# Kernel optimization log

Hardware: AMD Instinct MI355X
Metric: run time of the kernel (lower is better)

Reference implementation:

```python
import jax, jax.numpy as jnp
import numpy as np

B, L, E, H, D = 4, 4096, 1024, 16, 64  # batch, seq, embed, heads, head_dim
EPS = 1e-6


def setup_inputs() -> dict:
    key = jax.random.key(0)
    k1, k2, k3 = jax.random.split(key, 3)
    return {
        "q": jax.random.normal(k1, (B, L, E), dtype=jnp.float32),
        "k": jax.random.normal(k2, (B, L, E), dtype=jnp.float32),
        "v": jax.random.normal(k3, (B, L, E), dtype=jnp.float32),
        "mask": jnp.ones((B, L), dtype=jnp.float32),
    }


def _split_heads(x):
    # (B, L, E) -> (B*H, L, D)
    return x.reshape(B, L, H, D).transpose(0, 2, 1, 3).reshape(B * H, L, D)


def reference(q, k, v, mask):
    # feature map: relu
    q = jax.nn.relu(q)
    k = jax.nn.relu(k)
    # padding mask applied to keys/values
    k = k * mask[:, :, None]
    v = v * mask[:, :, None]
    q = _split_heads(q)
    k = _split_heads(k)
    v = _split_heads(v)
    # cosFormer sin/cos reweighting: pi/2 * i / m for i = 1..L
    idx = (np.pi / 2) * jnp.arange(1, L + 1, dtype=jnp.float32) / L
    s = jnp.sin(idx)[None, :, None]  # (1, L, 1)
    c = jnp.cos(idx)[None, :, None]
    q_ = jnp.concatenate([q * s, q * c], axis=-1)  # (B*H, L, 2D)
    k_ = jnp.concatenate([k * s, k * c], axis=-1)
    # linear-attention KV accumulation (non-causal): (B*H, 2D, D)
    kv = jnp.einsum('nld,nlm->ndm', k_, v)
    # normalizer
    z = 1.0 / jnp.maximum(jnp.einsum('nld,nd->nl', q_, k_.sum(axis=1)), EPS)
    out = jnp.einsum('nld,ndm,nl->nlm', q_, kv, z)  # (B*H, L, D)
    return out.reshape(B, H, L, D)
```

## Files before the change

### kernel.cpp

```cpp
#include <hip/hip_runtime.h>
#include <hip/hip_bf16.h>
#include <math.h>

#define B_ 4
#define L_ 4096
#define E_ 1024
#define H_ 16
#define D_ 64
#define N_ 64
#define D2_ 128
#define EPS_ 1e-6f

#define CH_ 16
#define LC_ (L_ / CH_)
#define LT_ 64

typedef short short8 __attribute__((ext_vector_type(8)));
typedef float f32x4 __attribute__((ext_vector_type(4)));
typedef unsigned int u32;
typedef unsigned short u16;

static __device__ __forceinline__ u32 pack2bf(float a, float b) {
  union { __hip_bfloat16 h; u16 s; } x, y;
  x.h = __float2bfloat16(a);
  y.h = __float2bfloat16(b);
  return (u32)x.s | ((u32)y.s << 16);
}

__global__ __launch_bounds__(256, 4) void phase1_mfma(
    const float* __restrict__ k, const float* __restrict__ v,
    const float* __restrict__ mask,
    float* __restrict__ part_kv, float* __restrict__ part_ks) {
  __shared__ __align__(16) u16 ka[D2_ * 72];
  __shared__ __align__(16) u16 vt[D_ * 72];
  __shared__ float msh[LT_], ssh[LT_], csh[LT_];

  const int bid = blockIdx.x;
  const int n = bid & 63;
  const int ch = bid >> 6;
  const int b = n >> 4;
  const int h = n & 15;
  const int t = threadIdx.x;
  const int wv = t >> 6;
  const int lane = t & 63;
  const int c_lo = lane & 15;
  const int lp = lane >> 4;
  const int c = wv * 16 + c_lo;

  f32x4 acc[2][4];
#pragma unroll
  for (int i = 0; i < 2; ++i)
#pragma unroll
    for (int j = 0; j < 4; ++j) acc[i][j] = (f32x4)0.f;
  float kss = 0.f, ksc = 0.f;

  const float angscale = 0.5f * 3.14159265358979f / (float)L_;

  for (int st = 0; st < LC_ / LT_; ++st) {
    const int l0 = ch * LC_ + st * LT_;
    __syncthreads();
    if (t < LT_) {
      const int gl = l0 + t;
      msh[t] = mask[b * L_ + gl];
      const float ang = (float)(gl + 1) * angscale;
      ssh[t] = __sinf(ang);
      csh[t] = __cosf(ang);
    }
    __syncthreads();
#pragma unroll
    for (int i = 0; i < 8; ++i) {
      const int l = 8 * i + 2 * lp;
      const size_t g0 = (size_t)(b * L_ + l0 + l) * E_ + h * 64 + c;
      const float k0 = k[g0], k1 = k[g0 + E_];
      const float v0 = v[g0], v1 = v[g0 + E_];
      const float m0 = msh[l], m1 = msh[l + 1];
      const float s0 = ssh[l], s1 = ssh[l + 1];
      const float c0 = csh[l], c1 = csh[l + 1];
      const float kr0 = fmaxf(k0, 0.f) * m0;
      const float kr1 = fmaxf(k1, 0.f) * m1;
      const float ks0 = kr0 * s0, ks1 = kr1 * s1;
      const float kc0 = kr0 * c0, kc1 = kr1 * c1;
      const int li = l >> 1;
      ((u32*)ka)[c * 36 + li]        = pack2bf(ks0, ks1);
      ((u32*)ka)[(c + 64) * 36 + li] = pack2bf(kc0, kc1);
      ((u32*)vt)[c * 36 + li]        = pack2bf(v0 * m0, v1 * m1);
      kss += ks0 + ks1;
      ksc += kc0 + kc1;
    }
    __syncthreads();
#pragma unroll
    for (int kk = 0; kk < 2; ++kk) {
      const int colo = kk * 32 + lp * 8;
      short8 af[2], bfr[4];
#pragma unroll
      for (int dt = 0; dt < 2; ++dt)
        af[dt] = *(const short8*)&ka[(wv * 32 + dt * 16 + c_lo) * 72 + colo];
#pragma unroll
      for (int mt = 0; mt < 4; ++mt)
        bfr[mt] = *(const short8*)&vt[(mt * 16 + c_lo) * 72 + colo];
#pragma unroll
      for (int dt = 0; dt < 2; ++dt)
#pragma unroll
        for (int mt = 0; mt < 4; ++mt)
          acc[dt][mt] = __builtin_amdgcn_mfma_f32_16x16x32_bf16(
              af[dt], bfr[mt], acc[dt][mt], 0, 0, 0);
    }
  }

  const size_t pbase = (size_t)(ch * N_ + n) * (D2_ * D_);
#pragma unroll
  for (int dt = 0; dt < 2; ++dt) {
    const int d = wv * 32 + dt * 16 + lp * 4;
#pragma unroll
    for (int mt = 0; mt < 4; ++mt) {
      const int mcol = mt * 16 + c_lo;
#pragma unroll
      for (int r = 0; r < 4; ++r)
        part_kv[pbase + (size_t)(d + r) * D_ + mcol] = acc[dt][mt][r];
    }
  }
  kss += __shfl_xor(kss, 16); kss += __shfl_xor(kss, 32);
  ksc += __shfl_xor(ksc, 16); ksc += __shfl_xor(ksc, 32);
  if (lp == 0) {
    part_ks[(size_t)(ch * N_ + n) * D2_ + c] = kss;
    part_ks[(size_t)(ch * N_ + n) * D2_ + c + 64] = ksc;
  }
}

__global__ __launch_bounds__(256) void reduce_t(
    const float* __restrict__ part_kv, const float* __restrict__ part_ks,
    u16* __restrict__ kvt, float* __restrict__ ks) {
  __shared__ float kvsh[D2_ * 65];
  const int n = blockIdx.x;
  const int t = threadIdx.x;

  for (int e = t; e < D2_ * D_; e += 256) {
    float s = 0.f;
#pragma unroll
    for (int cc = 0; cc < CH_; ++cc)
      s += part_kv[(size_t)(cc * N_ + n) * (D2_ * D_) + e];
    kvsh[(e >> 6) * 65 + (e & 63)] = s;
  }
  if (t < D2_) {
    float s = 0.f;
#pragma unroll
    for (int cc = 0; cc < CH_; ++cc)
      s += part_ks[(size_t)(cc * N_ + n) * D2_ + t];
    ks[n * D2_ + t] = s;
  }
  __syncthreads();
  for (int e = t; e < D2_ * D_; e += 256) {
    const int mcol = e >> 7, d = e & 127;
    union { __hip_bfloat16 h; u16 s; } cv;
    cv.h = __float2bfloat16(kvsh[d * 65 + mcol]);
    kvt[(size_t)n * (D2_ * D_) + (size_t)mcol * D2_ + d] = cv.s;
  }
}

__global__ __launch_bounds__(256, 4) void phase2_mfma(
    const float* __restrict__ q, const u16* __restrict__ kvt,
    const float* __restrict__ ks, float* __restrict__ out) {
  __shared__ __align__(16) u16 qa[64 * 136];
  __shared__ __align__(16) u16 kb[64 * 136];
  __shared__ __align__(16) u16 ksb[16 * 136];
  __shared__ float ssh[64], csh[64];

  const int bid = blockIdx.x;
  const int n = bid & 63;
  const int lc = bid >> 6;
  const int b = n >> 4, h = n & 15;
  const int t = threadIdx.x;
  const int wv = t >> 6, lane = t & 63;
  const int c_lo = lane & 15, quad = lane >> 4;
  const int l0 = lc * 64;

  if (t < 64) {
    const int gl = l0 + t;
    const float ang = (float)(gl + 1) * (0.5f * 3.14159265358979f / (float)L_);
    ssh[t] = __sinf(ang);
    csh[t] = __cosf(ang);
  }
  if (t < 68)
    ((u32*)ksb)[t] = (t < 64) ? pack2bf(ks[n * D2_ + 2 * t], ks[n * D2_ + 2 * t + 1]) : 0u;
  for (int i = 68 + t; i < 16 * 68; i += 256) ((u32*)ksb)[i] = 0u;
  {
    const u32* kv32 = (const u32*)(kvt + (size_t)n * (D2_ * D_));
#pragma unroll
    for (int i = 0; i < 16; ++i) {
      const int idx = t + 256 * i;
      ((u32*)kb)[(idx >> 6) * 68 + (idx & 63)] = kv32[idx];
    }
  }
  __syncthreads();

#pragma unroll
  for (int i = 0; i < 16; ++i) {
    const int l = wv + 4 * i;
    const int gl = l0 + l;
    float qv = q[(size_t)(b * L_ + gl) * E_ + h * 64 + lane];
    qv = fmaxf(qv, 0.f);
    const float qs = qv * ssh[l], qc = qv * csh[l];
    union { __hip_bfloat16 h; u16 s; } c1, c2;
    c1.h = __float2bfloat16(qs);
    c2.h = __float2bfloat16(qc);
    qa[l * 136 + lane] = c1.s;
    qa[l * 136 + lane + 64] = c2.s;
  }
  __syncthreads();

  f32x4 acc[4], acc5;
#pragma unroll
  for (int mt = 0; mt < 4; ++mt) acc[mt] = (f32x4)0.f;
  acc5 = (f32x4)0.f;

#pragma unroll
  for (int kk = 0; kk < 4; ++kk) {
    const int colo = kk * 32 + quad * 8;
    const short8 af = *(const short8*)&qa[(wv * 16 + c_lo) * 136 + colo];
#pragma unroll
    for (int mt = 0; mt < 4; ++mt) {
      const short8 bfr = *(const short8*)&kb[(mt * 16 + c_lo) * 136 + colo];
      acc[mt] = __builtin_amdgcn_mfma_f32_16x16x32_bf16(af, bfr, acc[mt], 0, 0, 0);
    }
    const short8 bks = *(const short8*)&ksb[c_lo * 136 + colo];
    acc5 = __builtin_amdgcn_mfma_f32_16x16x32_bf16(af, bks, acc5, 0, 0, 0);
  }

#pragma unroll
  for (int r = 0; r < 4; ++r) {
    const float den = __shfl(acc5[r], quad * 16);
    const float z = 1.f / fmaxf(den, EPS_);
    const int gl = l0 + wv * 16 + quad * 4 + r;
    const size_t ob = (size_t)n * (L_ * D_) + (size_t)gl * D_;
#pragma unroll
    for (int mt = 0; mt < 4; ++mt)
      out[ob + mt * 16 + c_lo] = acc[mt][r] * z;
  }
}

extern "C" void kernel_launch(void* const* d_in, const int* in_sizes, int n_in,
                              void* d_out, int out_size, void* d_ws,
                              size_t ws_size, hipStream_t stream) {
  const float* q = (const float*)d_in[0];
  const float* k = (const float*)d_in[1];
  const float* v = (const float*)d_in[2];
  const float* mask = (const float*)d_in[3];
  float* out = (float*)d_out;

  float* part_kv = (float*)d_ws;
  float* part_ks = part_kv + (size_t)CH_ * N_ * D2_ * D_;
  u16* kvt = (u16*)(part_ks + (size_t)CH_ * N_ * D2_);
  float* ks = (float*)(kvt + (size_t)N_ * D2_ * D_);

  phase1_mfma<<<dim3(CH_ * N_), dim3(256), 0, stream>>>(k, v, mask, part_kv, part_ks);
  reduce_t<<<dim3(N_), dim3(256), 0, stream>>>(part_kv, part_ks, kvt, ks);
  phase2_mfma<<<dim3(N_ * 64), dim3(256), 0, stream>>>(q, kvt, ks, out);
}
```

Baseline: 245.7 us.

## Prefetch phase1 loads in registers, parallelize reduce, drop LDS staging in phase2

Phase1 now uses half as many chunks and double-buffers the k/v global loads in registers, so the next tile is fetched while the current one is converted and multiplied. Sin/cos come from per-lane __sincosf and the mask from a wave shuffle, replacing the shared-memory tables. The reduce kernel is split eight ways per head with vectorized loads and packed stores to raise its parallelism. Phase2 builds its MFMA A and B fragments directly from global memory in registers with no LDS or barriers, at the cost of more redundant global reads of kvt and higher register pressure.

```diff
diff --git a/kernel.cpp b/kernel.cpp
--- a/kernel.cpp
+++ b/kernel.cpp
@@ -11,9 +11,12 @@
 #define D2_ 128
 #define EPS_ 1e-6f
 
-#define CH_ 16
+#define CH_ 8
 #define LC_ (L_ / CH_)
 #define LT_ 64
+#define NST_ (LC_ / LT_)
+
+#define DANG_ 3.83495197e-4f
 
 typedef short short8 __attribute__((ext_vector_type(8)));
 typedef float f32x4 __attribute__((ext_vector_type(4)));
@@ -27,13 +30,18 @@
   return (u32)x.s | ((u32)y.s << 16);
 }
 
-__global__ __launch_bounds__(256, 4) void phase1_mfma(
+static __device__ __forceinline__ short bf1(float a) {
+  union { __hip_bfloat16 h; short s; } x;
+  x.h = __float2bfloat16(a);
+  return x.s;
+}
+
+__global__ __launch_bounds__(256, 2) void phase1_mfma(
     const float* __restrict__ k, const float* __restrict__ v,
     const float* __restrict__ mask,
     float* __restrict__ part_kv, float* __restrict__ part_ks) {
   __shared__ __align__(16) u16 ka[D2_ * 72];
   __shared__ __align__(16) u16 vt[D_ * 72];
-  __shared__ float msh[LT_], ssh[LT_], csh[LT_];
 
   const int bid = blockIdx.x;
   const int n = bid & 63;
@@ -54,57 +62,77 @@
     for (int j = 0; j < 4; ++j) acc[i][j] = (f32x4)0.f;
   float kss = 0.f, ksc = 0.f;
 
-  const float angscale = 0.5f * 3.14159265358979f / (float)L_;
-
-  for (int st = 0; st < LC_ / LT_; ++st) {
-    const int l0 = ch * LC_ + st * LT_;
-    __syncthreads();
-    if (t < LT_) {
-      const int gl = l0 + t;
-      msh[t] = mask[b * L_ + gl];
-      const float ang = (float)(gl + 1) * angscale;
-      ssh[t] = __sinf(ang);
-      csh[t] = __cosf(ang);
-    }
-    __syncthreads();
-#pragma unroll
-    for (int i = 0; i < 8; ++i) {
-      const int l = 8 * i + 2 * lp;
-      const size_t g0 = (size_t)(b * L_ + l0 + l) * E_ + h * 64 + c;
-      const float k0 = k[g0], k1 = k[g0 + E_];
-      const float v0 = v[g0], v1 = v[g0 + E_];
-      const float m0 = msh[l], m1 = msh[l + 1];
-      const float s0 = ssh[l], s1 = ssh[l + 1];
-      const float c0 = csh[l], c1 = csh[l + 1];
-      const float kr0 = fmaxf(k0, 0.f) * m0;
-      const float kr1 = fmaxf(k1, 0.f) * m1;
-      const float ks0 = kr0 * s0, ks1 = kr1 * s1;
-      const float kc0 = kr0 * c0, kc1 = kr1 * c1;
-      const int li = l >> 1;
-      ((u32*)ka)[c * 36 + li]        = pack2bf(ks0, ks1);
-      ((u32*)ka)[(c + 64) * 36 + li] = pack2bf(kc0, kc1);
-      ((u32*)vt)[c * 36 + li]        = pack2bf(v0 * m0, v1 * m1);
-      kss += ks0 + ks1;
-      ksc += kc0 + kc1;
-    }
-    __syncthreads();
-#pragma unroll
-    for (int kk = 0; kk < 2; ++kk) {
-      const int colo = kk * 32 + lp * 8;
-      short8 af[2], bfr[4];
-#pragma unroll
-      for (int dt = 0; dt < 2; ++dt)
-        af[dt] = *(const short8*)&ka[(wv * 32 + dt * 16 + c_lo) * 72 + colo];
-#pragma unroll
-      for (int mt = 0; mt < 4; ++mt)
-        bfr[mt] = *(const short8*)&vt[(mt * 16 + c_lo) * 72 + colo];
-#pragma unroll
-      for (int dt = 0; dt < 2; ++dt)
-#pragma unroll
-        for (int mt = 0; mt < 4; ++mt)
-          acc[dt][mt] = __builtin_amdgcn_mfma_f32_16x16x32_bf16(
-              af[dt], bfr[mt], acc[dt][mt], 0, 0, 0);
-    }
+  const int l0 = ch * LC_;
+  const size_t gb0 = (size_t)(b * L_ + l0) * E_ + h * 64 + c;
+
+  float Ak0[8], Ak1[8], Av0[8], Av1[8], Am;
+  float Bk0[8], Bk1[8], Bv0[8], Bv1[8], Bm;
+
+#define P1_PREF(Rk0, Rk1, Rv0, Rv1, Rm, S)                                   \
+  do {                                                                       \
+    const size_t gs_ = gb0 + (size_t)(S) * (LT_ * E_);                       \
+    _Pragma("unroll") for (int i_ = 0; i_ < 8; ++i_) {                       \
+      const size_t g0_ = gs_ + (size_t)(8 * i_ + 2 * lp) * E_;               \
+      Rk0[i_] = k[g0_];                                                      \
+      Rk1[i_] = k[g0_ + E_];                                                 \
+      Rv0[i_] = v[g0_];                                                      \
+      Rv1[i_] = v[g0_ + E_];                                                 \
+    }                                                                        \
+    Rm = mask[(size_t)b * L_ + l0 + (S) * LT_ + lane];                       \
+  } while (0)
+
+#define P1_STAGE(Rk0, Rk1, Rv0, Rv1, Rm, S)                                  \
+  do {                                                                       \
+    const int lb_ = l0 + (S) * LT_;                                          \
+    _Pragma("unroll") for (int i_ = 0; i_ < 8; ++i_) {                       \
+      const int l_ = 8 * i_ + 2 * lp;                                        \
+      const float m0_ = __shfl(Rm, l_);                                      \
+      const float m1_ = __shfl(Rm, l_ + 1);                                  \
+      float s0_, c0_, s1_, c1_;                                              \
+      __sincosf((float)(lb_ + l_ + 1) * DANG_, &s0_, &c0_);                  \
+      __sincosf((float)(lb_ + l_ + 2) * DANG_, &s1_, &c1_);                  \
+      const float kr0_ = fmaxf(Rk0[i_], 0.f) * m0_;                          \
+      const float kr1_ = fmaxf(Rk1[i_], 0.f) * m1_;                          \
+      const float ks0_ = kr0_ * s0_, ks1_ = kr1_ * s1_;                      \
+      const float kc0_ = kr0_ * c0_, kc1_ = kr1_ * c1_;                      \
+      const int li_ = 4 * i_ + lp;                                           \
+      ((u32*)ka)[c * 36 + li_] = pack2bf(ks0_, ks1_);                        \
+      ((u32*)ka)[(c + 64) * 36 + li_] = pack2bf(kc0_, kc1_);                 \
+      ((u32*)vt)[c * 36 + li_] = pack2bf(Rv0[i_] * m0_, Rv1[i_] * m1_);      \
+      kss += ks0_ + ks1_;                                                    \
+      ksc += kc0_ + kc1_;                                                    \
+    }                                                                        \
+  } while (0)
+
+#define P1_MMA()                                                             \
+  do {                                                                       \
+    _Pragma("unroll") for (int kk_ = 0; kk_ < 2; ++kk_) {                    \
+      const int colo_ = kk_ * 32 + lp * 8;                                   \
+      short8 af_[2], bf_[4];                                                 \
+      _Pragma("unroll") for (int dt_ = 0; dt_ < 2; ++dt_)                    \
+          af_[dt_] =                                                         \
+              *(const short8*)&ka[(wv * 32 + dt_ * 16 + c_lo) * 72 + colo_]; \
+      _Pragma("unroll") for (int mt_ = 0; mt_ < 4; ++mt_)                    \
+          bf_[mt_] = *(const short8*)&vt[(mt_ * 16 + c_lo) * 72 + colo_];    \
+      _Pragma("unroll") for (int dt_ = 0; dt_ < 2; ++dt_)                    \
+          _Pragma("unroll") for (int mt_ = 0; mt_ < 4; ++mt_)                \
+              acc[dt_][mt_] = __builtin_amdgcn_mfma_f32_16x16x32_bf16(       \
+                  af_[dt_], bf_[mt_], acc[dt_][mt_], 0, 0, 0);               \
+    }                                                                        \
+  } while (0)
+
+  P1_PREF(Ak0, Ak1, Av0, Av1, Am, 0);
+  for (int st = 0; st < NST_; st += 2) {
+    __syncthreads();
+    P1_PREF(Bk0, Bk1, Bv0, Bv1, Bm, st + 1);
+    P1_STAGE(Ak0, Ak1, Av0, Av1, Am, st);
+    __syncthreads();
+    P1_MMA();
+    __syncthreads();
+    if (st + 2 < NST_) P1_PREF(Ak0, Ak1, Av0, Av1, Am, st + 2);
+    P1_STAGE(Bk0, Bk1, Bv0, Bv1, Bm, st + 1);
+    __syncthreads();
+    P1_MMA();
   }
 
   const size_t pbase = (size_t)(ch * N_ + n) * (D2_ * D_);
@@ -130,41 +158,39 @@
 __global__ __launch_bounds__(256) void reduce_t(
     const float* __restrict__ part_kv, const float* __restrict__ part_ks,
     u16* __restrict__ kvt, float* __restrict__ ks) {
-  __shared__ float kvsh[D2_ * 65];
-  const int n = blockIdx.x;
+  __shared__ __align__(16) float tsh[16 * 68];
+  const int bid = blockIdx.x;
+  const int n = bid >> 3;
+  const int sl = bid & 7;
   const int t = threadIdx.x;
 
-  for (int e = t; e < D2_ * D_; e += 256) {
-    float s = 0.f;
+  const int e0 = sl * 1024 + t * 4;
+  f32x4 s = (f32x4)0.f;
+#pragma unroll
+  for (int cc = 0; cc < CH_; ++cc)
+    s += *(const f32x4*)&part_kv[(size_t)(cc * N_ + n) * (D2_ * D_) + e0];
+  *(f32x4*)&tsh[(t >> 4) * 68 + (t & 15) * 4] = s;
+
+  if (sl == 0 && t < D2_) {
+    float ss = 0.f;
 #pragma unroll
     for (int cc = 0; cc < CH_; ++cc)
-      s += part_kv[(size_t)(cc * N_ + n) * (D2_ * D_) + e];
-    kvsh[(e >> 6) * 65 + (e & 63)] = s;
-  }
-  if (t < D2_) {
-    float s = 0.f;
-#pragma unroll
-    for (int cc = 0; cc < CH_; ++cc)
-      s += part_ks[(size_t)(cc * N_ + n) * D2_ + t];
-    ks[n * D2_ + t] = s;
+      ss += part_ks[(size_t)(cc * N_ + n) * D2_ + t];
+    ks[n * D2_ + t] = ss;
   }
   __syncthreads();
-  for (int e = t; e < D2_ * D_; e += 256) {
-    const int mcol = e >> 7, d = e & 127;
-    union { __hip_bfloat16 h; u16 s; } cv;
-    cv.h = __float2bfloat16(kvsh[d * 65 + mcol]);
-    kvt[(size_t)n * (D2_ * D_) + (size_t)mcol * D2_ + d] = cv.s;
-  }
+
+  const int m = t >> 2;
+  const int d4 = (t & 3) * 4;
+  const u32 lo = pack2bf(tsh[(d4 + 0) * 68 + m], tsh[(d4 + 1) * 68 + m]);
+  const u32 hi = pack2bf(tsh[(d4 + 2) * 68 + m], tsh[(d4 + 3) * 68 + m]);
+  uint2 pk; pk.x = lo; pk.y = hi;
+  *(uint2*)&kvt[(size_t)n * (D2_ * D_) + (size_t)m * D2_ + sl * 16 + d4] = pk;
 }
 
 __global__ __launch_bounds__(256, 4) void phase2_mfma(
     const float* __restrict__ q, const u16* __restrict__ kvt,
     const float* __restrict__ ks, float* __restrict__ out) {
-  __shared__ __align__(16) u16 qa[64 * 136];
-  __shared__ __align__(16) u16 kb[64 * 136];
-  __shared__ __align__(16) u16 ksb[16 * 136];
-  __shared__ float ssh[64], csh[64];
-
   const int bid = blockIdx.x;
   const int n = bid & 63;
   const int lc = bid >> 6;
@@ -173,57 +199,62 @@
   const int wv = t >> 6, lane = t & 63;
   const int c_lo = lane & 15, quad = lane >> 4;
   const int l0 = lc * 64;
-
-  if (t < 64) {
-    const int gl = l0 + t;
-    const float ang = (float)(gl + 1) * (0.5f * 3.14159265358979f / (float)L_);
-    ssh[t] = __sinf(ang);
-    csh[t] = __cosf(ang);
-  }
-  if (t < 68)
-    ((u32*)ksb)[t] = (t < 64) ? pack2bf(ks[n * D2_ + 2 * t], ks[n * D2_ + 2 * t + 1]) : 0u;
-  for (int i = 68 + t; i < 16 * 68; i += 256) ((u32*)ksb)[i] = 0u;
-  {
-    const u32* kv32 = (const u32*)(kvt + (size_t)n * (D2_ * D_));
-#pragma unroll
-    for (int i = 0; i < 16; ++i) {
-      const int idx = t + 256 * i;
-      ((u32*)kb)[(idx >> 6) * 68 + (idx & 63)] = kv32[idx];
+  const int row = l0 + wv * 16 + c_lo;
+
+  const float* qr = q + (size_t)(b * L_ + row) * E_ + h * 64;
+  const f32x4 q0 = *(const f32x4*)(qr + quad * 8);
+  const f32x4 q1 = *(const f32x4*)(qr + quad * 8 + 4);
+  const f32x4 q2 = *(const f32x4*)(qr + 32 + quad * 8);
+  const f32x4 q3 = *(const f32x4*)(qr + 32 + quad * 8 + 4);
+
+  float sv, cv;
+  __sincosf((float)(row + 1) * DANG_, &sv, &cv);
+
+  short8 af[4];
+#pragma unroll
+  for (int j = 0; j < 4; ++j) {
+    const float a = fmaxf(q0[j], 0.f);
+    const float e = fmaxf(q1[j], 0.f);
+    const float f = fmaxf(q2[j], 0.f);
+    const float g = fmaxf(q3[j], 0.f);
+    af[0][j] = bf1(a * sv); af[0][j + 4] = bf1(e * sv);
+    af[1][j] = bf1(f * sv); af[1][j + 4] = bf1(g * sv);
+    af[2][j] = bf1(a * cv); af[2][j + 4] = bf1(e * cv);
+    af[3][j] = bf1(f * cv); af[3][j + 4] = bf1(g * cv);
+  }
+
+  const float* ksn = ks + n * D2_;
+  short8 bks[4];
+#pragma unroll
+  for (int kk = 0; kk < 4; ++kk) {
+    const f32x4 ka_ = *(const f32x4*)(ksn + kk * 32 + quad * 8);
+    const f32x4 kb_ = *(const f32x4*)(ksn + kk * 32 + quad * 8 + 4);
+    short8 tt = {0, 0, 0, 0, 0, 0, 0, 0};
+    if (c_lo == 0) {
+#pragma unroll
+      for (int j = 0; j < 4; ++j) {
+        tt[j] = bf1(ka_[j]);
+        tt[j + 4] = bf1(kb_[j]);
+      }
     }
-  }
-  __syncthreads();
-
-#pragma unroll
-  for (int i = 0; i < 16; ++i) {
-    const int l = wv + 4 * i;
-    const int gl = l0 + l;
-    float qv = q[(size_t)(b * L_ + gl) * E_ + h * 64 + lane];
-    qv = fmaxf(qv, 0.f);
-    const float qs = qv * ssh[l], qc = qv * csh[l];
-    union { __hip_bfloat16 h; u16 s; } c1, c2;
-    c1.h = __float2bfloat16(qs);
-    c2.h = __float2bfloat16(qc);
-    qa[l * 136 + lane] = c1.s;
-    qa[l * 136 + lane + 64] = c2.s;
-  }
-  __syncthreads();
-
-  f32x4 acc[4], acc5;
+    bks[kk] = tt;
+  }
+
+  const u16* kvh = kvt + (size_t)n * (D2_ * D_);
+  f32x4 acc[4];
 #pragma unroll
   for (int mt = 0; mt < 4; ++mt) acc[mt] = (f32x4)0.f;
-  acc5 = (f32x4)0.f;
+  f32x4 acc5 = (f32x4)0.f;
 
 #pragma unroll
   for (int kk = 0; kk < 4; ++kk) {
-    const int colo = kk * 32 + quad * 8;
-    const short8 af = *(const short8*)&qa[(wv * 16 + c_lo) * 136 + colo];
 #pragma unroll
     for (int mt = 0; mt < 4; ++mt) {
-      const short8 bfr = *(const short8*)&kb[(mt * 16 + c_lo) * 136 + colo];
-      acc[mt] = __builtin_amdgcn_mfma_f32_16x16x32_bf16(af, bfr, acc[mt], 0, 0, 0);
+      const short8 bfr =
+          *(const short8*)&kvh[(mt * 16 + c_lo) * D2_ + kk * 32 + quad * 8];
+      acc[mt] = __builtin_amdgcn_mfma_f32_16x16x32_bf16(af[kk], bfr, acc[mt], 0, 0, 0);
     }
-    const short8 bks = *(const short8*)&ksb[c_lo * 136 + colo];
-    acc5 = __builtin_amdgcn_mfma_f32_16x16x32_bf16(af, bks, acc5, 0, 0, 0);
+    acc5 = __builtin_amdgcn_mfma_f32_16x16x32_bf16(af[kk], bks[kk], acc5, 0, 0, 0);
   }
 
 #pragma unroll
@@ -253,6 +284,6 @@
   float* ks = (float*)(kvt + (size_t)N_ * D2_ * D_);
 
   phase1_mfma<<<dim3(CH_ * N_), dim3(256), 0, stream>>>(k, v, mask, part_kv, part_ks);
-  reduce_t<<<dim3(N_), dim3(256), 0, stream>>>(part_kv, part_ks, kvt, ks);
+  reduce_t<<<dim3(N_ * 8), dim3(256), 0, stream>>>(part_kv, part_ks, kvt, ks);
   phase2_mfma<<<dim3(N_ * 64), dim3(256), 0, stream>>>(q, kvt, ks, out);
 }
```

Result: slower. 265.6 us (+8.1%).
